# Kernel optimization log

Hardware: AMD Instinct MI355X
Metric: run time of the kernel (lower is better)

The kernel has to match this reference:

```python
import jax, jax.numpy as jnp
import numpy as np

B = 131072
IN = 128
H = 128

def setup_inputs() -> dict:
    key = jax.random.key(0)
    ks = jax.random.split(key, 12)
    # kaiming-normal-ish init for weights (std ~ sqrt(2/fan_out))
    std_w = (2.0 / H) ** 0.5
    inp = {
        'x': jax.random.normal(ks[0], (B, IN), dtype=jnp.float32),
        'h_prev': jax.random.normal(ks[1], (B, H), dtype=jnp.float32),
        'c_prev': jax.random.normal(ks[2], (B, H), dtype=jnp.float32),
        'Wi': jax.random.normal(ks[3], (IN, H), dtype=jnp.float32) * std_w,
        'Ui': jax.random.normal(ks[4], (H, H), dtype=jnp.float32) * std_w,
        'bi': jnp.ones((H,), dtype=jnp.float32),
        'Wf': jax.random.normal(ks[5], (IN, H), dtype=jnp.float32) * std_w,
        'Uf': jax.random.normal(ks[6], (H, H), dtype=jnp.float32) * std_w,
        'bf': jnp.ones((H,), dtype=jnp.float32),
        'Wg': jax.random.normal(ks[7], (IN, H), dtype=jnp.float32) * std_w,
        'Ug': jax.random.normal(ks[8], (H, H), dtype=jnp.float32) * std_w,
        'bg': jnp.ones((H,), dtype=jnp.float32),
        'Wo': jax.random.normal(ks[9], (IN, H), dtype=jnp.float32) * std_w,
        'Uo': jax.random.normal(ks[10], (H, H), dtype=jnp.float32) * std_w,
        'bo': jnp.ones((H,), dtype=jnp.float32),
    }
    return inp

def reference(x, h_prev, c_prev, Wi, Ui, bi, Wf, Uf, bf, Wg, Ug, bg, Wo, Uo, bo):
    # Faithful per-gate math (i, f, o sigmoid gates; g tanh candidate)
    ig = jax.nn.sigmoid(x @ Wi + h_prev @ Ui + bi)
    fg = jax.nn.sigmoid(x @ Wf + h_prev @ Uf + bf)
    og = jax.nn.sigmoid(x @ Wo + h_prev @ Uo + bo)
    cc = jnp.tanh(x @ Wg + h_prev @ Ug + bg)
    c = fg * c_prev + ig * cc
    h = og * jnp.tanh(c)
    return (h, c)
```

## Files before the change

kernel.cpp:

```cpp
#include <hip/hip_runtime.h>


#define B_ROWS 131072
#define HDIM 128
#define KDIM 256
#define BM 32
#define LDT 132

typedef __attribute__((ext_vector_type(4))) float f32x4;
typedef __attribute__((ext_vector_type(8))) short s16x8;

__device__ inline unsigned short f2bf(float f) {
    unsigned int u = __float_as_uint(f);
    u += 0x7fffu + ((u >> 16) & 1u);
    return (unsigned short)(u >> 16);
}

__device__ inline float frcp(float x) { return __builtin_amdgcn_rcpf(x); }
__device__ inline float fsigmoid(float x) { return frcp(1.0f + __expf(-x)); }
__device__ inline float ftanh(float x) { return 1.0f - 2.0f * frcp(__expf(2.0f * x) + 1.0f); }

__global__ void prep_weights(const float* __restrict__ Wi, const float* __restrict__ Ui,
                             const float* __restrict__ Wf, const float* __restrict__ Uf,
                             const float* __restrict__ Wg, const float* __restrict__ Ug,
                             const float* __restrict__ Wo, const float* __restrict__ Uo,
                             unsigned short* __restrict__ Bp) {
    int idx = blockIdx.x * 256 + threadIdx.x;
    int e   = idx & 7;
    int q   = (idx >> 3) & 3;
    int t16 = (idx >> 5) & 15;
    int ni  = (idx >> 9) & 3;
    int kc  = (idx >> 11) & 7;
    int w   = idx >> 14;
    int j = w * 16 + t16;
    int k = kc * 32 + q * 8 + e;
    const float* Wp = ni == 0 ? Wi : ni == 1 ? Wf : ni == 2 ? Wg : Wo;
    const float* Up = ni == 0 ? Ui : ni == 1 ? Uf : ni == 2 ? Ug : Uo;
    float v = (k < 128) ? Wp[k * HDIM + j] : Up[(k - 128) * HDIM + j];
    Bp[idx] = f2bf(v);
}

__global__ __launch_bounds__(512, 6) void lstm_main(
    const float* __restrict__ x, const float* __restrict__ h_prev,
    const float* __restrict__ c_prev,
    const unsigned short* __restrict__ Bp,
    const float* __restrict__ bi, const float* __restrict__ bf_,
    const float* __restrict__ bg, const float* __restrict__ bo,
    float* __restrict__ out)
{
    __shared__ float smem[2 * BM * LDT];
    float* hbuf = smem;
    float* cbuf = smem + BM * LDT;
    unsigned short* As = (unsigned short*)smem;

    const int tid = threadIdx.x;
    const int m0 = blockIdx.x * BM;

    float4 cpv[2];
    #pragma unroll
    for (int it = 0; it < 2; ++it) {
        int f = it * 512 + tid;
        int r = f >> 5, c4 = f & 31;
        cpv[it] = *(const float4*)(c_prev + (size_t)(m0 + r) * HDIM + c4 * 4);
    }

    #pragma unroll
    for (int it = 0; it < 4; ++it) {
        int fi = it * 512 + tid;
        int r  = fi >> 6;
        int c4 = fi & 63;
        int k0 = c4 * 4;
        const float* src = (k0 < 128) ? (x + (size_t)(m0 + r) * HDIM + k0)
                                      : (h_prev + (size_t)(m0 + r) * HDIM + (k0 - 128));
        float4 v = *(const float4*)src;
        ushort4 p;
        p.x = f2bf(v.x); p.y = f2bf(v.y); p.z = f2bf(v.z); p.w = f2bf(v.w);
        int mi = r >> 4, t16r = r & 15;
        int kc = k0 >> 5, qq = (k0 >> 3) & 3, e0 = k0 & 7;
        *(ushort4*)&As[((mi * 8 + kc) * 16 + t16r) * 32 + qq * 8 + e0] = p;
    }

    #pragma unroll
    for (int it = 0; it < 2; ++it) {
        int f = it * 512 + tid;
        int r = f >> 5, c4 = f & 31;
        *(float4*)&cbuf[r * LDT + c4 * 4] = cpv[it];
    }
    __syncthreads();

    const int wave = tid >> 6;
    const int lane = tid & 63;
    const int t16 = lane & 15;
    const int q = lane >> 4;
    const int lane_off = t16 * 32 + q * 8;

    f32x4 acc[2][4];
    const f32x4 zero = {0.0f, 0.0f, 0.0f, 0.0f};
    #pragma unroll
    for (int mi = 0; mi < 2; ++mi)
        #pragma unroll
        for (int ni = 0; ni < 4; ++ni)
            acc[mi][ni] = zero;

    const unsigned short* bbase = Bp + (size_t)(wave * 8) * 2048 + lane_off;

    #pragma unroll
    for (int kc = 0; kc < 8; ++kc) {
        s16x8 a[2], b[4];
        #pragma unroll
        for (int ni = 0; ni < 4; ++ni)
            b[ni] = *(const s16x8*)(bbase + kc * 2048 + ni * 512);
        #pragma unroll
        for (int mi = 0; mi < 2; ++mi)
            a[mi] = *(const s16x8*)&As[(mi * 8 + kc) * 512 + lane_off];
        #pragma unroll
        for (int mi = 0; mi < 2; ++mi)
            #pragma unroll
            for (int ni = 0; ni < 4; ++ni)
                acc[mi][ni] = __builtin_amdgcn_mfma_f32_16x16x32_bf16(a[mi], b[ni], acc[mi][ni], 0, 0, 0);
    }
    __syncthreads();

    const int j = wave * 16 + t16;
    const float vbi = bi[j], vbf = bf_[j], vbg = bg[j], vbo = bo[j];

    #pragma unroll
    for (int mi = 0; mi < 2; ++mi) {
        #pragma unroll
        for (int r = 0; r < 4; ++r) {
            int rt = mi * 16 + q * 4 + r;
            float cp = cbuf[rt * LDT + j];
            float ig = fsigmoid(acc[mi][0][r] + vbi);
            float fg = fsigmoid(acc[mi][1][r] + vbf);
            float cc = ftanh(acc[mi][2][r] + vbg);
            float og = fsigmoid(acc[mi][3][r] + vbo);
            float c = fg * cp + ig * cc;
            float h = og * ftanh(c);
            hbuf[rt * LDT + j] = h;
            cbuf[rt * LDT + j] = c;
        }
    }
    __syncthreads();

    float* hout = out;
    float* cout = out + (size_t)B_ROWS * HDIM;
    #pragma unroll
    for (int it = 0; it < 2; ++it) {
        int f = it * 512 + tid;
        int r = f >> 5, c4 = f & 31;
        size_t goff = (size_t)(m0 + r) * HDIM + c4 * 4;
        *(float4*)(hout + goff) = *(const float4*)&hbuf[r * LDT + c4 * 4];
        *(float4*)(cout + goff) = *(const float4*)&cbuf[r * LDT + c4 * 4];
    }
}

extern "C" void kernel_launch(void* const* d_in, const int* in_sizes, int n_in,
                              void* d_out, int out_size, void* d_ws, size_t ws_size,
                              hipStream_t stream) {
    const float* x      = (const float*)d_in[0];
    const float* h_prev = (const float*)d_in[1];
    const float* c_prev = (const float*)d_in[2];
    const float* Wi = (const float*)d_in[3];
    const float* Ui = (const float*)d_in[4];
    const float* bi = (const float*)d_in[5];
    const float* Wf = (const float*)d_in[6];
    const float* Uf = (const float*)d_in[7];
    const float* bf = (const float*)d_in[8];
    const float* Wg = (const float*)d_in[9];
    const float* Ug = (const float*)d_in[10];
    const float* bg = (const float*)d_in[11];
    const float* Wo = (const float*)d_in[12];
    const float* Uo = (const float*)d_in[13];
    const float* bo = (const float*)d_in[14];

    unsigned short* Bp = (unsigned short*)d_ws;

    prep_weights<<<512, 256, 0, stream>>>(Wi, Ui, Wf, Uf, Wg, Ug, Wo, Uo, Bp);
    lstm_main<<<B_ROWS / BM, 512, 0, stream>>>(x, h_prev, c_prev, Bp, bi, bf, bg, bo, (float*)d_out);
}
```

Measured before the change: 330.0 us.

## Make LSTM kernel persistent with double-buffered prefetch of next row tile

The main kernel now launches a fixed 512 blocks, each looping over 8 consecutive 32-row tiles. While one tile's MFMA and gate math run, the next tile's x, h_prev and c_prev are loaded into registers, then converted to bf16 and written into a second LDS buffer. This is meant to hide global-load latency behind compute and to amortize per-block setup such as bias loads. In exchange LDS use and register pressure go up, the occupancy hint drops from 6 to 4, and with only 512 blocks there may be fewer waves in flight to hide latency.

```diff
diff --git a/kernel.cpp b/kernel.cpp
--- a/kernel.cpp
+++ b/kernel.cpp
@@ -3,9 +3,10 @@
 
 #define B_ROWS 131072
 #define HDIM 128
-#define KDIM 256
 #define BM 32
 #define LDT 132
+#define NBLK 512
+#define TPB 8
 
 typedef __attribute__((ext_vector_type(4))) float f32x4;
 typedef __attribute__((ext_vector_type(8))) short s16x8;
@@ -40,7 +41,7 @@
     Bp[idx] = f2bf(v);
 }
 
-__global__ __launch_bounds__(512, 6) void lstm_main(
+__global__ __launch_bounds__(512, 4) void lstm_main(
     const float* __restrict__ x, const float* __restrict__ h_prev,
     const float* __restrict__ c_prev,
     const unsigned short* __restrict__ Bp,
@@ -48,109 +49,149 @@
     const float* __restrict__ bg, const float* __restrict__ bo,
     float* __restrict__ out)
 {
-    __shared__ float smem[2 * BM * LDT];
-    float* hbuf = smem;
-    float* cbuf = smem + BM * LDT;
-    unsigned short* As = (unsigned short*)smem;
+    __shared__ float smem[8192 + 2 * BM * LDT];
+    unsigned short* As0 = (unsigned short*)smem;
+    unsigned short* As1 = (unsigned short*)(smem + 4096);
+    float* cbuf = smem + 8192;
+    float* hbuf = smem + 8192 + BM * LDT;
 
     const int tid = threadIdx.x;
-    const int m0 = blockIdx.x * BM;
-
-    float4 cpv[2];
-    #pragma unroll
-    for (int it = 0; it < 2; ++it) {
-        int f = it * 512 + tid;
-        int r = f >> 5, c4 = f & 31;
-        cpv[it] = *(const float4*)(c_prev + (size_t)(m0 + r) * HDIM + c4 * 4);
-    }
-
-    #pragma unroll
-    for (int it = 0; it < 4; ++it) {
-        int fi = it * 512 + tid;
-        int r  = fi >> 6;
-        int c4 = fi & 63;
-        int k0 = c4 * 4;
-        const float* src = (k0 < 128) ? (x + (size_t)(m0 + r) * HDIM + k0)
-                                      : (h_prev + (size_t)(m0 + r) * HDIM + (k0 - 128));
-        float4 v = *(const float4*)src;
-        ushort4 p;
-        p.x = f2bf(v.x); p.y = f2bf(v.y); p.z = f2bf(v.z); p.w = f2bf(v.w);
-        int mi = r >> 4, t16r = r & 15;
-        int kc = k0 >> 5, qq = (k0 >> 3) & 3, e0 = k0 & 7;
-        *(ushort4*)&As[((mi * 8 + kc) * 16 + t16r) * 32 + qq * 8 + e0] = p;
-    }
-
-    #pragma unroll
-    for (int it = 0; it < 2; ++it) {
-        int f = it * 512 + tid;
-        int r = f >> 5, c4 = f & 31;
-        *(float4*)&cbuf[r * LDT + c4 * 4] = cpv[it];
-    }
-    __syncthreads();
-
     const int wave = tid >> 6;
     const int lane = tid & 63;
     const int t16 = lane & 15;
     const int q = lane >> 4;
     const int lane_off = t16 * 32 + q * 8;
 
-    f32x4 acc[2][4];
-    const f32x4 zero = {0.0f, 0.0f, 0.0f, 0.0f};
-    #pragma unroll
-    for (int mi = 0; mi < 2; ++mi)
-        #pragma unroll
-        for (int ni = 0; ni < 4; ++ni)
-            acc[mi][ni] = zero;
-
+    const int tile0 = blockIdx.x * TPB;
+
+    const int j = wave * 16 + t16;
+    const float vbi = bi[j], vbf = bf_[j], vbg = bg[j], vbo = bo[j];
     const unsigned short* bbase = Bp + (size_t)(wave * 8) * 2048 + lane_off;
-
-    #pragma unroll
-    for (int kc = 0; kc < 8; ++kc) {
-        s16x8 a[2], b[4];
-        #pragma unroll
-        for (int ni = 0; ni < 4; ++ni)
-            b[ni] = *(const s16x8*)(bbase + kc * 2048 + ni * 512);
-        #pragma unroll
-        for (int mi = 0; mi < 2; ++mi)
-            a[mi] = *(const s16x8*)&As[(mi * 8 + kc) * 512 + lane_off];
-        #pragma unroll
-        for (int mi = 0; mi < 2; ++mi)
-            #pragma unroll
-            for (int ni = 0; ni < 4; ++ni)
-                acc[mi][ni] = __builtin_amdgcn_mfma_f32_16x16x32_bf16(a[mi], b[ni], acc[mi][ni], 0, 0, 0);
+    float* hout = out;
+    float* cout = out + (size_t)B_ROWS * HDIM;
+
+    float4 sv[4], cv[2];
+
+    {
+        const int m0 = tile0 * BM;
+        #pragma unroll
+        for (int it = 0; it < 4; ++it) {
+            int fi = it * 512 + tid; int r = fi >> 6; int c4 = fi & 63; int k0 = c4 * 4;
+            const float* src = (k0 < 128) ? (x + (size_t)(m0 + r) * HDIM + k0)
+                                          : (h_prev + (size_t)(m0 + r) * HDIM + (k0 - 128));
+            sv[it] = *(const float4*)src;
+        }
+        #pragma unroll
+        for (int it = 0; it < 2; ++it) {
+            int f = it * 512 + tid; int r = f >> 5; int c4 = f & 31;
+            cv[it] = *(const float4*)(c_prev + (size_t)(m0 + r) * HDIM + c4 * 4);
+        }
+        #pragma unroll
+        for (int it = 0; it < 4; ++it) {
+            int fi = it * 512 + tid; int r = fi >> 6; int c4 = fi & 63; int k0 = c4 * 4;
+            ushort4 p;
+            p.x = f2bf(sv[it].x); p.y = f2bf(sv[it].y); p.z = f2bf(sv[it].z); p.w = f2bf(sv[it].w);
+            int mi = r >> 4, t16r = r & 15;
+            int kc = k0 >> 5, qq = (k0 >> 3) & 3, e0 = k0 & 7;
+            *(ushort4*)&As0[((mi * 8 + kc) * 16 + t16r) * 32 + qq * 8 + e0] = p;
+        }
+        #pragma unroll
+        for (int it = 0; it < 2; ++it) {
+            int f = it * 512 + tid; int r = f >> 5; int c4 = f & 31;
+            *(float4*)&cbuf[r * LDT + c4 * 4] = cv[it];
+        }
     }
     __syncthreads();
 
-    const int j = wave * 16 + t16;
-    const float vbi = bi[j], vbf = bf_[j], vbg = bg[j], vbo = bo[j];
-
-    #pragma unroll
-    for (int mi = 0; mi < 2; ++mi) {
-        #pragma unroll
-        for (int r = 0; r < 4; ++r) {
-            int rt = mi * 16 + q * 4 + r;
-            float cp = cbuf[rt * LDT + j];
-            float ig = fsigmoid(acc[mi][0][r] + vbi);
-            float fg = fsigmoid(acc[mi][1][r] + vbf);
-            float cc = ftanh(acc[mi][2][r] + vbg);
-            float og = fsigmoid(acc[mi][3][r] + vbo);
-            float c = fg * cp + ig * cc;
-            float h = og * ftanh(c);
-            hbuf[rt * LDT + j] = h;
-            cbuf[rt * LDT + j] = c;
-        }
-    }
-    __syncthreads();
-
-    float* hout = out;
-    float* cout = out + (size_t)B_ROWS * HDIM;
-    #pragma unroll
-    for (int it = 0; it < 2; ++it) {
-        int f = it * 512 + tid;
-        int r = f >> 5, c4 = f & 31;
-        size_t goff = (size_t)(m0 + r) * HDIM + c4 * 4;
-        *(float4*)(hout + goff) = *(const float4*)&hbuf[r * LDT + c4 * 4];
-        *(float4*)(cout + goff) = *(const float4*)&cbuf[r * LDT + c4 * 4];
+    #pragma unroll 2
+    for (int t = 0; t < TPB; ++t) {
+        const unsigned short* Ac = (t & 1) ? As1 : As0;
+        unsigned short* An = (t & 1) ? As0 : As1;
+        const bool have_next = (t + 1 < TPB);
+
+        if (have_next) {
+            const int m0n = (tile0 + t + 1) * BM;
+            #pragma unroll
+            for (int it = 0; it < 4; ++it) {
+                int fi = it * 512 + tid; int r = fi >> 6; int c4 = fi & 63; int k0 = c4 * 4;
+                const float* src = (k0 < 128) ? (x + (size_t)(m0n + r) * HDIM + k0)
+                                              : (h_prev + (size_t)(m0n + r) * HDIM + (k0 - 128));
+                sv[it] = *(const float4*)src;
+            }
+            #pragma unroll
+            for (int it = 0; it < 2; ++it) {
+                int f = it * 512 + tid; int r = f >> 5; int c4 = f & 31;
+                cv[it] = *(const float4*)(c_prev + (size_t)(m0n + r) * HDIM + c4 * 4);
+            }
+        }
+
+        f32x4 acc[2][4];
+        const f32x4 zero = {0.0f, 0.0f, 0.0f, 0.0f};
+        #pragma unroll
+        for (int mi = 0; mi < 2; ++mi)
+            #pragma unroll
+            for (int ni = 0; ni < 4; ++ni)
+                acc[mi][ni] = zero;
+
+        #pragma unroll
+        for (int kc = 0; kc < 8; ++kc) {
+            s16x8 a[2], b[4];
+            #pragma unroll
+            for (int ni = 0; ni < 4; ++ni)
+                b[ni] = *(const s16x8*)(bbase + kc * 2048 + ni * 512);
+            #pragma unroll
+            for (int mi = 0; mi < 2; ++mi)
+                a[mi] = *(const s16x8*)&Ac[(mi * 8 + kc) * 512 + lane_off];
+            #pragma unroll
+            for (int mi = 0; mi < 2; ++mi)
+                #pragma unroll
+                for (int ni = 0; ni < 4; ++ni)
+                    acc[mi][ni] = __builtin_amdgcn_mfma_f32_16x16x32_bf16(a[mi], b[ni], acc[mi][ni], 0, 0, 0);
+        }
+
+        #pragma unroll
+        for (int mi = 0; mi < 2; ++mi) {
+            #pragma unroll
+            for (int r = 0; r < 4; ++r) {
+                int rt = mi * 16 + q * 4 + r;
+                float cp = cbuf[rt * LDT + j];
+                float ig = fsigmoid(acc[mi][0][r] + vbi);
+                float fg = fsigmoid(acc[mi][1][r] + vbf);
+                float cc = ftanh(acc[mi][2][r] + vbg);
+                float og = fsigmoid(acc[mi][3][r] + vbo);
+                float c = fg * cp + ig * cc;
+                float h = og * ftanh(c);
+                hbuf[rt * LDT + j] = h;
+                cbuf[rt * LDT + j] = c;
+            }
+        }
+        __syncthreads();
+
+        {
+            const int m0c = (tile0 + t) * BM;
+            #pragma unroll
+            for (int it = 0; it < 2; ++it) {
+                int f = it * 512 + tid; int r = f >> 5; int c4 = f & 31;
+                size_t goff = (size_t)(m0c + r) * HDIM + c4 * 4;
+                float4 cc4 = *(const float4*)&cbuf[r * LDT + c4 * 4];
+                *(float4*)(cout + goff) = cc4;
+                if (have_next)
+                    *(float4*)&cbuf[r * LDT + c4 * 4] = cv[it];
+                *(float4*)(hout + goff) = *(const float4*)&hbuf[r * LDT + c4 * 4];
+            }
+            if (have_next) {
+                #pragma unroll
+                for (int it = 0; it < 4; ++it) {
+                    int fi = it * 512 + tid; int r = fi >> 6; int c4 = fi & 63; int k0 = c4 * 4;
+                    ushort4 p;
+                    p.x = f2bf(sv[it].x); p.y = f2bf(sv[it].y); p.z = f2bf(sv[it].z); p.w = f2bf(sv[it].w);
+                    int mi = r >> 4, t16r = r & 15;
+                    int kc = k0 >> 5, qq = (k0 >> 3) & 3, e0 = k0 & 7;
+                    *(ushort4*)&An[((mi * 8 + kc) * 16 + t16r) * 32 + qq * 8 + e0] = p;
+                }
+            }
+        }
+        __syncthreads();
     }
 }
 
@@ -176,5 +217,5 @@
     unsigned short* Bp = (unsigned short*)d_ws;
 
     prep_weights<<<512, 256, 0, stream>>>(Wi, Ui, Wf, Uf, Wg, Ug, Wo, Uo, Bp);
-    lstm_main<<<B_ROWS / BM, 512, 0, stream>>>(x, h_prev, c_prev, Bp, bi, bf, bg, bo, (float*)d_out);
-}
+    lstm_main<<<NBLK, 512, 0, stream>>>(x, h_prev, c_prev, Bp, bi, bf, bg, bo, (float*)d_out);
+}
```

Result: slower. 462.9 us (+40.3%).

## Swap MFMA operands so accumulators map to contiguous columns, store directly

Applied to the files above, without the earlier changes.

Swaps the A and B roles in the MFMA so weights are the row operand and activations the column operand. Each lane's accumulator registers then hold four consecutive hidden columns of one batch row. That lets c_prev be read and h/c written as float4 straight from registers, which removes the shared-memory staging buffers and two barriers. It also shrinks LDS to just the bf16 activation tile and lowers the occupancy hint from 6 to 4. The risk is that the direct per-lane stores are 16-byte chunks spread over rows, which coalesce less well than full-row stores.

```diff
diff --git a/kernel.cpp b/kernel.cpp
--- a/kernel.cpp
+++ b/kernel.cpp
@@ -3,9 +3,7 @@
 
 #define B_ROWS 131072
 #define HDIM 128
-#define KDIM 256
 #define BM 32
-#define LDT 132
 
 typedef __attribute__((ext_vector_type(4))) float f32x4;
 typedef __attribute__((ext_vector_type(8))) short s16x8;
@@ -40,7 +38,7 @@
     Bp[idx] = f2bf(v);
 }
 
-__global__ __launch_bounds__(512, 6) void lstm_main(
+__global__ __launch_bounds__(512, 4) void lstm_main(
     const float* __restrict__ x, const float* __restrict__ h_prev,
     const float* __restrict__ c_prev,
     const unsigned short* __restrict__ Bp,
@@ -48,21 +46,15 @@
     const float* __restrict__ bg, const float* __restrict__ bo,
     float* __restrict__ out)
 {
-    __shared__ float smem[2 * BM * LDT];
-    float* hbuf = smem;
-    float* cbuf = smem + BM * LDT;
-    unsigned short* As = (unsigned short*)smem;
+    __shared__ unsigned short Bs[8192];
 
     const int tid = threadIdx.x;
     const int m0 = blockIdx.x * BM;
-
-    float4 cpv[2];
-    #pragma unroll
-    for (int it = 0; it < 2; ++it) {
-        int f = it * 512 + tid;
-        int r = f >> 5, c4 = f & 31;
-        cpv[it] = *(const float4*)(c_prev + (size_t)(m0 + r) * HDIM + c4 * 4);
-    }
+    const int wave = tid >> 6;
+    const int lane = tid & 63;
+    const int t16 = lane & 15;
+    const int q = lane >> 4;
+    const int lane_off = t16 * 32 + q * 8;
 
     #pragma unroll
     for (int it = 0; it < 4; ++it) {
@@ -77,80 +69,70 @@
         p.x = f2bf(v.x); p.y = f2bf(v.y); p.z = f2bf(v.z); p.w = f2bf(v.w);
         int mi = r >> 4, t16r = r & 15;
         int kc = k0 >> 5, qq = (k0 >> 3) & 3, e0 = k0 & 7;
-        *(ushort4*)&As[((mi * 8 + kc) * 16 + t16r) * 32 + qq * 8 + e0] = p;
-    }
-
-    #pragma unroll
-    for (int it = 0; it < 2; ++it) {
-        int f = it * 512 + tid;
-        int r = f >> 5, c4 = f & 31;
-        *(float4*)&cbuf[r * LDT + c4 * 4] = cpv[it];
+        *(ushort4*)&Bs[((mi * 8 + kc) * 16 + t16r) * 32 + qq * 8 + e0] = p;
     }
     __syncthreads();
 
-    const int wave = tid >> 6;
-    const int lane = tid & 63;
-    const int t16 = lane & 15;
-    const int q = lane >> 4;
-    const int lane_off = t16 * 32 + q * 8;
+    const unsigned short* abase = Bp + (size_t)wave * 16384 + lane_off;
 
-    f32x4 acc[2][4];
+    f32x4 acc[4][2];
     const f32x4 zero = {0.0f, 0.0f, 0.0f, 0.0f};
     #pragma unroll
-    for (int mi = 0; mi < 2; ++mi)
+    for (int g = 0; g < 4; ++g)
         #pragma unroll
-        for (int ni = 0; ni < 4; ++ni)
-            acc[mi][ni] = zero;
-
-    const unsigned short* bbase = Bp + (size_t)(wave * 8) * 2048 + lane_off;
+        for (int mi = 0; mi < 2; ++mi)
+            acc[g][mi] = zero;
 
     #pragma unroll
     for (int kc = 0; kc < 8; ++kc) {
-        s16x8 a[2], b[4];
-        #pragma unroll
-        for (int ni = 0; ni < 4; ++ni)
-            b[ni] = *(const s16x8*)(bbase + kc * 2048 + ni * 512);
+        s16x8 b[2], a[4];
         #pragma unroll
         for (int mi = 0; mi < 2; ++mi)
-            a[mi] = *(const s16x8*)&As[(mi * 8 + kc) * 512 + lane_off];
+            b[mi] = *(const s16x8*)&Bs[(mi * 8 + kc) * 512 + lane_off];
         #pragma unroll
-        for (int mi = 0; mi < 2; ++mi)
+        for (int g = 0; g < 4; ++g)
+            a[g] = *(const s16x8*)(abase + kc * 2048 + g * 512);
+        #pragma unroll
+        for (int g = 0; g < 4; ++g)
             #pragma unroll
-            for (int ni = 0; ni < 4; ++ni)
-                acc[mi][ni] = __builtin_amdgcn_mfma_f32_16x16x32_bf16(a[mi], b[ni], acc[mi][ni], 0, 0, 0);
+            for (int mi = 0; mi < 2; ++mi)
+                acc[g][mi] = __builtin_amdgcn_mfma_f32_16x16x32_bf16(a[g], b[mi], acc[g][mi], 0, 0, 0);
     }
-    __syncthreads();
 
-    const int j = wave * 16 + t16;
-    const float vbi = bi[j], vbf = bf_[j], vbg = bg[j], vbo = bo[j];
+    const int jv = wave * 16 + q * 4;
+    const float4 vbi = *(const float4*)(bi + jv);
+    const float4 vbf = *(const float4*)(bf_ + jv);
+    const float4 vbg = *(const float4*)(bg + jv);
+    const float4 vbo = *(const float4*)(bo + jv);
+
+    float* hout = out;
+    float* cout = out + (size_t)B_ROWS * HDIM;
 
     #pragma unroll
     for (int mi = 0; mi < 2; ++mi) {
+        const size_t moff = (size_t)(m0 + mi * 16 + t16) * HDIM + jv;
+        float4 cp = *(const float4*)(c_prev + moff);
+        float4 hv, cv;
         #pragma unroll
         for (int r = 0; r < 4; ++r) {
-            int rt = mi * 16 + q * 4 + r;
-            float cp = cbuf[rt * LDT + j];
-            float ig = fsigmoid(acc[mi][0][r] + vbi);
-            float fg = fsigmoid(acc[mi][1][r] + vbf);
-            float cc = ftanh(acc[mi][2][r] + vbg);
-            float og = fsigmoid(acc[mi][3][r] + vbo);
-            float c = fg * cp + ig * cc;
+            float bi_r = r == 0 ? vbi.x : r == 1 ? vbi.y : r == 2 ? vbi.z : vbi.w;
+            float bf_r = r == 0 ? vbf.x : r == 1 ? vbf.y : r == 2 ? vbf.z : vbf.w;
+            float bg_r = r == 0 ? vbg.x : r == 1 ? vbg.y : r == 2 ? vbg.z : vbg.w;
+            float bo_r = r == 0 ? vbo.x : r == 1 ? vbo.y : r == 2 ? vbo.z : vbo.w;
+            float cp_r = r == 0 ? cp.x : r == 1 ? cp.y : r == 2 ? cp.z : cp.w;
+            float ig = fsigmoid(acc[0][mi][r] + bi_r);
+            float fg = fsigmoid(acc[1][mi][r] + bf_r);
+            float cc = ftanh(acc[2][mi][r] + bg_r);
+            float og = fsigmoid(acc[3][mi][r] + bo_r);
+            float c = fg * cp_r + ig * cc;
             float h = og * ftanh(c);
-            hbuf[rt * LDT + j] = h;
-            cbuf[rt * LDT + j] = c;
+            if (r == 0) { hv.x = h; cv.x = c; }
+            else if (r == 1) { hv.y = h; cv.y = c; }
+            else if (r == 2) { hv.z = h; cv.z = c; }
+            else { hv.w = h; cv.w = c; }
         }
-    }
-    __syncthreads();
-
-    float* hout = out;
-    float* cout = out + (size_t)B_ROWS * HDIM;
-    #pragma unroll
-    for (int it = 0; it < 2; ++it) {
-        int f = it * 512 + tid;
-        int r = f >> 5, c4 = f & 31;
-        size_t goff = (size_t)(m0 + r) * HDIM + c4 * 4;
-        *(float4*)(hout + goff) = *(const float4*)&hbuf[r * LDT + c4 * 4];
-        *(float4*)(cout + goff) = *(const float4*)&cbuf[r * LDT + c4 * 4];
+        *(float4*)(hout + moff) = hv;
+        *(float4*)(cout + moff) = cv;
     }
 }
 
```

Result: slower. 345.8 us (+4.8%).
